# Kernel optimization log

Measured on AMD Instinct MI355X. Metric: run time of the kernel, lower is better.

The kernel has to match this reference:

```python
import jax, jax.numpy as jnp
import numpy as np

NUM_HEADS = 8
QK_DIM = 64
V_DIM = 64


def _conv1x1(W, b, x):
    # W: [out, in], x: [N, in, T, V] -> [N, out, T, V]
    return jnp.einsum('oc,nctv->notv', W, x) + b[None, :, None, None]


def setup_inputs() -> dict:
    key = jax.random.key(0)
    ks = jax.random.split(key, 10)
    N, C, T, V = 8, 256, 1024, 25
    s = 0.02
    return {
        'feature': jax.random.normal(ks[0], (N, C, T, V), jnp.float32),
        'text_feature': jax.random.normal(ks[1], (1, 512, 1, V), jnp.float32),
        'Wq': jax.random.normal(ks[2], (NUM_HEADS * QK_DIM, 512), jnp.float32) * s,
        'bq': jax.random.normal(ks[3], (NUM_HEADS * QK_DIM,), jnp.float32) * s,
        'Wk': jax.random.normal(ks[4], (NUM_HEADS * QK_DIM, 512), jnp.float32) * s,
        'bk': jax.random.normal(ks[5], (NUM_HEADS * QK_DIM,), jnp.float32) * s,
        'Wv': jax.random.normal(ks[6], (V_DIM, C), jnp.float32) * s,
        'bv': jax.random.normal(ks[7], (V_DIM,), jnp.float32) * s,
        'Wo': jax.random.normal(ks[8], (C, NUM_HEADS * V_DIM), jnp.float32) * s,
        'bo': jax.random.normal(ks[9], (C,), jnp.float32) * s,
    }


def reference(feature, text_feature, Wq, bq, Wk, bk, Wv, bv, Wo, bo):
    N, C, T, V = feature.shape
    tf = jnp.broadcast_to(text_feature, (N, 512, 1, V))  # expand over batch
    # Q/K from text features (T dim collapses to 1)
    q = _conv1x1(Wq, bq, tf).reshape(N, NUM_HEADS, QK_DIM, V)
    k = _conv1x1(Wk, bk, tf).reshape(N, NUM_HEADS, QK_DIM, V)
    v = _conv1x1(Wv, bv, feature)  # [N, v_dim, T, V]
    energy = jnp.einsum('nhcu,nhcv->nhuv', q, k) / jnp.sqrt(jnp.float32(QK_DIM))
    attn = jax.nn.softmax(energy, axis=-1)  # [N, H, V, V]
    z = jnp.einsum('nctu,nhuv->nhctv', v, attn).reshape(N, NUM_HEADS * V_DIM, T, V)
    out = _conv1x1(Wo, bo, z) + feature
    return out
```

## Files before the change

kernel.cpp:

```cpp
#include <hip/hip_runtime.h>
#include <hip/hip_bf16.h>


typedef __attribute__((ext_vector_type(8))) short short8;
typedef __attribute__((ext_vector_type(4))) float f4v;

static __device__ __forceinline__ unsigned short f2bf(float f) {
  union { float f; unsigned u; } v; v.f = f;
  unsigned r = v.u + 0x7fffu + ((v.u >> 16) & 1u);
  return (unsigned short)(r >> 16);
}
static __device__ __forceinline__ float bf2f(unsigned short h) {
  union { unsigned u; float f; } v; v.u = ((unsigned)h) << 16;
  return v.f;
}


__global__ void k_qk_conv(const float* __restrict__ tf,
                          const float* __restrict__ Wq, const float* __restrict__ bq,
                          const float* __restrict__ Wk, const float* __restrict__ bk,
                          const float* __restrict__ Wv, const float* __restrict__ Wo,
                          unsigned short* __restrict__ WvP,
                          unsigned short* __restrict__ WoP,
                          float* __restrict__ qkP)
{
  __shared__ float tfl[12800];
  const int b = blockIdx.x, tid = threadIdx.x;
  if (b < 100) {
    for (int i = tid; i < 12800; i += 256) tfl[i] = tf[i];
    __syncthreads();
    int idx = b * 256 + tid;
    int isK = idx >= 12800;
    int j = isK ? idx - 12800 : idx;
    int g = j / 25, u = j - 25 * g;
    const float* wrow = (isK ? Wk : Wq) + g * 512;
    float s = (isK ? bk : bq)[g];
    for (int i = 0; i < 512; ++i) s += wrow[i] * tfl[i * 25 + u];
    qkP[idx] = s;
  } else {
    int cb = b - 100;
    for (int i = cb * 256 + tid; i < 16896; i += 64 * 256) {
      int c = i / 264, kk = i - 264 * c;
      WvP[i] = (kk < 256) ? f2bf(Wv[c * 256 + kk]) : (unsigned short)0;
    }
    for (int i = cb * 256 + tid; i < 147456; i += 64 * 256) {
      int hh = i / 18432, rr = i - 18432 * hh;
      int o = rr / 72, kk = rr - 72 * o;
      WoP[i] = (kk < 64) ? f2bf(Wo[o * 512 + hh * 64 + kk]) : (unsigned short)0;
    }
  }
}

__global__ void k_attn(const float* __restrict__ qkP,
                       unsigned short* __restrict__ attnP)
{
  __shared__ float ql[1600], kl[1600], attl[625];
  const int h = blockIdx.x, tid = threadIdx.x;
  for (int i = tid; i < 1600; i += 256) {
    ql[i] = qkP[h * 1600 + i];
    kl[i] = qkP[12800 + h * 1600 + i];
  }
  __syncthreads();
  if (tid < 25) {
    int u = tid;
    float e[25];
    float mx = -1e30f;
    #pragma unroll
    for (int v = 0; v < 25; ++v) {
      float s = 0.f;
      #pragma unroll
      for (int r = 0; r < 64; ++r) s += ql[r * 25 + u] * kl[r * 25 + v];
      s *= 0.125f;
      e[v] = s;
      mx = fmaxf(mx, s);
    }
    float den = 0.f;
    #pragma unroll
    for (int v = 0; v < 25; ++v) { e[v] = __expf(e[v] - mx); den += e[v]; }
    float inv = 1.f / den;
    #pragma unroll
    for (int v = 0; v < 25; ++v) attl[u * 25 + v] = e[v] * inv;
  }
  __syncthreads();
  for (int i = tid; i < 1280; i += 256) {
    int vp = i / 40, u = i - 40 * vp;
    attnP[h * 1280 + i] =
        (vp < 25 && u < 25) ? f2bf(attl[u * 25 + vp]) : (unsigned short)0;
  }
}

__launch_bounds__(512, 2)
__global__ void k_main(const float* __restrict__ feature,
                       const float* __restrict__ bv,
                       const float* __restrict__ bo,
                       const unsigned short* __restrict__ WvP,
                       const unsigned short* __restrict__ WoP,
                       const unsigned short* __restrict__ attnP,
                       float* __restrict__ out)
{
  extern __shared__ char smem[];
  unsigned short* Fl = (unsigned short*)smem;
  unsigned short* Vl = (unsigned short*)(smem + 67584);
  unsigned short* Zl = (unsigned short*)(smem + 84992);
  unsigned short* Wl = (unsigned short*)(smem + 103424);

  const int tid  = threadIdx.x;
  const int wave = tid >> 6;
  const int lane = tid & 63;
  const int quad = lane >> 4;
  const int l16  = lane & 15;
  const int n  = blockIdx.x >> 8;
  const int tb = blockIdx.x & 255;
  const int t0 = tb * 4;

  {
    short8 z = {0, 0, 0, 0, 0, 0, 0, 0};
    short8* fz = (short8*)smem;
    for (int i = tid; i < 4224; i += 512) fz[i] = z;
  }
  __syncthreads();

  {
    const int c = tid >> 1, p = tid & 1;
    const float4* src = reinterpret_cast<const float4*>(
        feature + ((size_t)(n * 256 + c) * 1024 + t0) * 25);
    for (int i = p; i < 25; i += 2) {
      float4 f = src[i];
      float vv[4] = {f.x, f.y, f.z, f.w};
      int j0 = 4 * i;
      #pragma unroll
      for (int e = 0; e < 4; ++e) {
        int j = j0 + e;
        int t = j / 25;
        int vp = j - 25 * t;
        Fl[(t * 32 + vp) * 264 + c] = f2bf(vv[e]);
      }
    }
  }
  __syncthreads();

  const int wm = wave >> 1, wn = wave & 1;

  f4v acc[4][4];
  #pragma unroll
  for (int mi = 0; mi < 4; ++mi) {
    #pragma unroll
    for (int r = 0; r < 4; ++r) {
      int o = wm * 64 + mi * 16 + quad * 4 + r;
      float bor = bo[o];
      #pragma unroll
      for (int ni = 0; ni < 4; ++ni) {
        int colb = wn * 64 + ni * 16 + l16;
        acc[mi][ni][r] = bor + bf2f(Fl[colb * 264 + o]);
      }
    }
  }

  {
    const int mt1 = wave & 3, nh1 = wave >> 2;
    f4v accv[4];
    #pragma unroll
    for (int ni = 0; ni < 4; ++ni) {
      #pragma unroll
      for (int r = 0; r < 4; ++r) accv[ni][r] = bv[mt1 * 16 + quad * 4 + r];
    }
    #pragma unroll
    for (int ks = 0; ks < 8; ++ks) {
      short8 a = *reinterpret_cast<const short8*>(
          WvP + (mt1 * 16 + l16) * 264 + ks * 32 + quad * 8);
      #pragma unroll
      for (int ni = 0; ni < 4; ++ni) {
        int colb = (4 * nh1 + ni) * 16 + l16;
        short8 b = *reinterpret_cast<const short8*>(
            &Fl[colb * 264 + ks * 32 + quad * 8]);
        accv[ni] = __builtin_amdgcn_mfma_f32_16x16x32_bf16(a, b, accv[ni], 0, 0, 0);
      }
    }
    #pragma unroll
    for (int ni = 0; ni < 4; ++ni) {
      int colb = (4 * nh1 + ni) * 16 + l16;
      #pragma unroll
      for (int r = 0; r < 4; ++r) {
        int c = mt1 * 16 + quad * 4 + r;
        Vl[c * 136 + colb] = f2bf(accv[ni][r]);
      }
    }
  }
  __syncthreads();

  #pragma unroll 1
  for (int h = 0; h < 8; ++h) {
    const short8* wsrc = reinterpret_cast<const short8*>(WoP + h * 18432);
    short8 wo_stage[5];
    #pragma unroll
    for (int c2 = 0; c2 < 5; ++c2) {
      int i = tid + c2 * 512;
      if (i < 2304) wo_stage[c2] = wsrc[i];
    }

    {
      const int t2 = wave >> 1, mh = wave & 1;
      f4v accz[2][2];
      #pragma unroll
      for (int m2 = 0; m2 < 2; ++m2) {
        #pragma unroll
        for (int n2 = 0; n2 < 2; ++n2) {
          f4v z = {0.f, 0.f, 0.f, 0.f};
          accz[m2][n2] = z;
        }
      }
      short8 bfrag[2];
      #pragma unroll
      for (int n2 = 0; n2 < 2; ++n2)
        bfrag[n2] = *reinterpret_cast<const short8*>(
            attnP + h * 1280 + (n2 * 16 + l16) * 40 + quad * 8);
      #pragma unroll
      for (int m2 = 0; m2 < 2; ++m2) {
        short8 a = *reinterpret_cast<const short8*>(
            &Vl[((2 * mh + m2) * 16 + l16) * 136 + t2 * 32 + quad * 8]);
        #pragma unroll
        for (int n2 = 0; n2 < 2; ++n2)
          accz[m2][n2] =
              __builtin_amdgcn_mfma_f32_16x16x32_bf16(a, bfrag[n2], accz[m2][n2], 0, 0, 0);
      }
      #pragma unroll
      for (int m2 = 0; m2 < 2; ++m2) {
        #pragma unroll
        for (int n2 = 0; n2 < 2; ++n2) {
          #pragma unroll
          for (int r = 0; r < 4; ++r) {
            int c = (2 * mh + m2) * 16 + quad * 4 + r;
            int colz = t2 * 32 + n2 * 16 + l16;
            Zl[colz * 72 + c] = f2bf(accz[m2][n2][r]);
          }
        }
      }
    }

    {
      short8* wdst = reinterpret_cast<short8*>(Wl);
      #pragma unroll
      for (int c2 = 0; c2 < 5; ++c2) {
        int i = tid + c2 * 512;
        if (i < 2304) wdst[i] = wo_stage[c2];
      }
    }
    __syncthreads();

    #pragma unroll
    for (int ks = 0; ks < 2; ++ks) {
      short8 afr[4], bfr[4];
      #pragma unroll
      for (int mi = 0; mi < 4; ++mi)
        afr[mi] = *reinterpret_cast<const short8*>(
            &Wl[(wm * 64 + mi * 16 + l16) * 72 + ks * 32 + quad * 8]);
      #pragma unroll
      for (int ni = 0; ni < 4; ++ni)
        bfr[ni] = *reinterpret_cast<const short8*>(
            &Zl[(wn * 64 + ni * 16 + l16) * 72 + ks * 32 + quad * 8]);
      #pragma unroll
      for (int mi = 0; mi < 4; ++mi) {
        #pragma unroll
        for (int ni = 0; ni < 4; ++ni)
          acc[mi][ni] =
              __builtin_amdgcn_mfma_f32_16x16x32_bf16(afr[mi], bfr[ni], acc[mi][ni], 0, 0, 0);
      }
    }
    __syncthreads();
  }

  #pragma unroll
  for (int ni = 0; ni < 4; ++ni) {
    int colb = wn * 64 + ni * 16 + l16;
    int t = colb >> 5, vp = colb & 31;
    if (vp < 25) {
      #pragma unroll
      for (int mi = 0; mi < 4; ++mi) {
        #pragma unroll
        for (int r = 0; r < 4; ++r) {
          int o = wm * 64 + mi * 16 + quad * 4 + r;
          out[((size_t)(n * 256 + o) * 1024 + (t0 + t)) * 25 + vp] = acc[mi][ni][r];
        }
      }
    }
  }
}

extern "C" void kernel_launch(void* const* d_in, const int* in_sizes, int n_in,
                              void* d_out, int out_size, void* d_ws, size_t ws_size,
                              hipStream_t stream)
{
  const float* feature = (const float*)d_in[0];
  const float* tf      = (const float*)d_in[1];
  const float* Wq      = (const float*)d_in[2];
  const float* bq      = (const float*)d_in[3];
  const float* Wk      = (const float*)d_in[4];
  const float* bk      = (const float*)d_in[5];
  const float* Wv      = (const float*)d_in[6];
  const float* bv      = (const float*)d_in[7];
  const float* Wo      = (const float*)d_in[8];
  const float* bo      = (const float*)d_in[9];
  float* out = (float*)d_out;

  unsigned short* WvP   = (unsigned short*)d_ws;
  unsigned short* WoP   = WvP + 16896;
  unsigned short* attnP = WoP + 147456;
  float* qkP = (float*)(attnP + 10240);

  hipLaunchKernelGGL(k_qk_conv, dim3(164), dim3(256), 0, stream,
                     tf, Wq, bq, Wk, bk, Wv, Wo, WvP, WoP, qkP);
  hipLaunchKernelGGL(k_attn, dim3(8), dim3(256), 0, stream, qkP, attnP);

  hipFuncSetAttribute(reinterpret_cast<const void*>(&k_main),
                      hipFuncAttributeMaxDynamicSharedMemorySize, 140288);
  hipLaunchKernelGGL(k_main, dim3(2048), dim3(512), 140288, stream,
                     feature, bv, bo, WvP, WoP, attnP, out);
}
```

Measured before the change: 551.2 us.

## Halve per-block time tile and read Wo fragments straight from global

The main kernel now processes 2 time steps per block instead of 4, doubling the grid and shrinking LDS use from about 140KB to about 52KB so more blocks can be resident per CU (launch bounds raised to 6). The per-head Wo staging through shared memory is removed and the MFMA A fragments are loaded directly from the packed bf16 Wo in global/L2, with padding dropped from the Wv/Wo packed layouts. This aims to raise occupancy and remove an LDS copy and its register staging. In exchange, Wo is re-read from cache by twice as many blocks, and the unpadded global loads rely on L2 bandwidth.

```diff
diff --git a/kernel.cpp b/kernel.cpp
--- a/kernel.cpp
+++ b/kernel.cpp
@@ -3,6 +3,7 @@
 
 
 typedef __attribute__((ext_vector_type(8))) short short8;
+typedef __attribute__((ext_vector_type(4))) short short4v;
 typedef __attribute__((ext_vector_type(4))) float f4v;
 
 static __device__ __forceinline__ unsigned short f2bf(float f) {
@@ -39,14 +40,13 @@
     qkP[idx] = s;
   } else {
     int cb = b - 100;
-    for (int i = cb * 256 + tid; i < 16896; i += 64 * 256) {
-      int c = i / 264, kk = i - 264 * c;
-      WvP[i] = (kk < 256) ? f2bf(Wv[c * 256 + kk]) : (unsigned short)0;
-    }
-    for (int i = cb * 256 + tid; i < 147456; i += 64 * 256) {
-      int hh = i / 18432, rr = i - 18432 * hh;
-      int o = rr / 72, kk = rr - 72 * o;
-      WoP[i] = (kk < 64) ? f2bf(Wo[o * 512 + hh * 64 + kk]) : (unsigned short)0;
+    for (int i = cb * 256 + tid; i < 16384; i += 64 * 256) {
+      WvP[i] = f2bf(Wv[i]);
+    }
+    for (int i = cb * 256 + tid; i < 131072; i += 64 * 256) {
+      int hh = i >> 14, rr = i & 16383;
+      int o = rr >> 6, kk = rr & 63;
+      WoP[i] = f2bf(Wo[o * 512 + hh * 64 + kk]);
     }
   }
 }
@@ -89,7 +89,7 @@
   }
 }
 
-__launch_bounds__(512, 2)
+__launch_bounds__(512, 6)
 __global__ void k_main(const float* __restrict__ feature,
                        const float* __restrict__ bv,
                        const float* __restrict__ bo,
@@ -100,57 +100,54 @@
 {
   extern __shared__ char smem[];
   unsigned short* Fl = (unsigned short*)smem;
-  unsigned short* Vl = (unsigned short*)(smem + 67584);
-  unsigned short* Zl = (unsigned short*)(smem + 84992);
-  unsigned short* Wl = (unsigned short*)(smem + 103424);
+  unsigned short* Vl = (unsigned short*)(smem + 33792);
+  unsigned short* Zl = (unsigned short*)(smem + 43008);
 
   const int tid  = threadIdx.x;
   const int wave = tid >> 6;
   const int lane = tid & 63;
   const int quad = lane >> 4;
   const int l16  = lane & 15;
-  const int n  = blockIdx.x >> 8;
-  const int tb = blockIdx.x & 255;
-  const int t0 = tb * 4;
+  const int n  = blockIdx.x >> 9;
+  const int tb = blockIdx.x & 511;
+  const int t0 = tb * 2;
 
   {
     short8 z = {0, 0, 0, 0, 0, 0, 0, 0};
     short8* fz = (short8*)smem;
-    for (int i = tid; i < 4224; i += 512) fz[i] = z;
+    for (int i = tid; i < 2112; i += 512) fz[i] = z;
   }
   __syncthreads();
 
   {
     const int c = tid >> 1, p = tid & 1;
-    const float4* src = reinterpret_cast<const float4*>(
+    const float2* src = reinterpret_cast<const float2*>(
         feature + ((size_t)(n * 256 + c) * 1024 + t0) * 25);
     for (int i = p; i < 25; i += 2) {
-      float4 f = src[i];
-      float vv[4] = {f.x, f.y, f.z, f.w};
-      int j0 = 4 * i;
-      #pragma unroll
-      for (int e = 0; e < 4; ++e) {
-        int j = j0 + e;
-        int t = j / 25;
-        int vp = j - 25 * t;
-        Fl[(t * 32 + vp) * 264 + c] = f2bf(vv[e]);
-      }
-    }
-  }
-  __syncthreads();
-
-  const int wm = wave >> 1, wn = wave & 1;
-
-  f4v acc[4][4];
+      float2 f = src[i];
+      int j0 = 2 * i;
+      {
+        int j = j0;       int t = (j >= 25); int vp = j - 25 * t;
+        Fl[(t * 32 + vp) * 264 + c] = f2bf(f.x);
+      }
+      {
+        int j = j0 + 1;   int t = (j >= 25); int vp = j - 25 * t;
+        Fl[(t * 32 + vp) * 264 + c] = f2bf(f.y);
+      }
+    }
+  }
+  __syncthreads();
+
+  f4v acc[2][4];
   #pragma unroll
-  for (int mi = 0; mi < 4; ++mi) {
+  for (int mi = 0; mi < 2; ++mi) {
     #pragma unroll
     for (int r = 0; r < 4; ++r) {
-      int o = wm * 64 + mi * 16 + quad * 4 + r;
+      int o = wave * 32 + mi * 16 + quad * 4 + r;
       float bor = bo[o];
       #pragma unroll
       for (int ni = 0; ni < 4; ++ni) {
-        int colb = wn * 64 + ni * 16 + l16;
+        int colb = ni * 16 + l16;
         acc[mi][ni][r] = bor + bf2f(Fl[colb * 264 + o]);
       }
     }
@@ -158,31 +155,31 @@
 
   {
     const int mt1 = wave & 3, nh1 = wave >> 2;
-    f4v accv[4];
-    #pragma unroll
-    for (int ni = 0; ni < 4; ++ni) {
+    f4v accv[2];
+    #pragma unroll
+    for (int ni = 0; ni < 2; ++ni) {
       #pragma unroll
       for (int r = 0; r < 4; ++r) accv[ni][r] = bv[mt1 * 16 + quad * 4 + r];
     }
     #pragma unroll
     for (int ks = 0; ks < 8; ++ks) {
       short8 a = *reinterpret_cast<const short8*>(
-          WvP + (mt1 * 16 + l16) * 264 + ks * 32 + quad * 8);
-      #pragma unroll
-      for (int ni = 0; ni < 4; ++ni) {
-        int colb = (4 * nh1 + ni) * 16 + l16;
+          WvP + (mt1 * 16 + l16) * 256 + ks * 32 + quad * 8);
+      #pragma unroll
+      for (int ni = 0; ni < 2; ++ni) {
+        int colb = (2 * nh1 + ni) * 16 + l16;
         short8 b = *reinterpret_cast<const short8*>(
             &Fl[colb * 264 + ks * 32 + quad * 8]);
         accv[ni] = __builtin_amdgcn_mfma_f32_16x16x32_bf16(a, b, accv[ni], 0, 0, 0);
       }
     }
     #pragma unroll
-    for (int ni = 0; ni < 4; ++ni) {
-      int colb = (4 * nh1 + ni) * 16 + l16;
+    for (int ni = 0; ni < 2; ++ni) {
+      int colb = (2 * nh1 + ni) * 16 + l16;
       #pragma unroll
       for (int r = 0; r < 4; ++r) {
         int c = mt1 * 16 + quad * 4 + r;
-        Vl[c * 136 + colb] = f2bf(accv[ni][r]);
+        Vl[c * 72 + colb] = f2bf(accv[ni][r]);
       }
     }
   }
@@ -190,80 +187,51 @@
 
   #pragma unroll 1
   for (int h = 0; h < 8; ++h) {
-    const short8* wsrc = reinterpret_cast<const short8*>(WoP + h * 18432);
-    short8 wo_stage[5];
-    #pragma unroll
-    for (int c2 = 0; c2 < 5; ++c2) {
-      int i = tid + c2 * 512;
-      if (i < 2304) wo_stage[c2] = wsrc[i];
-    }
-
     {
-      const int t2 = wave >> 1, mh = wave & 1;
-      f4v accz[2][2];
-      #pragma unroll
-      for (int m2 = 0; m2 < 2; ++m2) {
-        #pragma unroll
-        for (int n2 = 0; n2 < 2; ++n2) {
-          f4v z = {0.f, 0.f, 0.f, 0.f};
-          accz[m2][n2] = z;
+      const int am = wave >> 1;
+      const int np = wave & 1;
+      short8 a = *reinterpret_cast<const short8*>(
+          &Vl[(am * 16 + l16) * 72 + np * 32 + quad * 8]);
+      f4v accz[2];
+      #pragma unroll
+      for (int j = 0; j < 2; ++j) {
+        f4v z = {0.f, 0.f, 0.f, 0.f};
+        short8 b = *reinterpret_cast<const short8*>(
+            attnP + h * 1280 + (j * 16 + l16) * 40 + quad * 8);
+        accz[j] = __builtin_amdgcn_mfma_f32_16x16x32_bf16(a, b, z, 0, 0, 0);
+      }
+      #pragma unroll
+      for (int j = 0; j < 2; ++j) {
+        int col = np * 32 + j * 16 + l16;
+        int c0 = am * 16 + quad * 4;
+        short4v zz;
+        #pragma unroll
+        for (int r = 0; r < 4; ++r) zz[r] = (short)f2bf(accz[j][r]);
+        *reinterpret_cast<short4v*>(&Zl[col * 72 + c0]) = zz;
+      }
+    }
+    __syncthreads();
+
+    {
+      const unsigned short* __restrict__ woh = WoP + h * 16384;
+      #pragma unroll
+      for (int ks = 0; ks < 2; ++ks) {
+        short8 bfr[4], afr[2];
+        #pragma unroll
+        for (int ni = 0; ni < 4; ++ni)
+          bfr[ni] = *reinterpret_cast<const short8*>(
+              &Zl[(ni * 16 + l16) * 72 + ks * 32 + quad * 8]);
+        #pragma unroll
+        for (int mi = 0; mi < 2; ++mi)
+          afr[mi] = *reinterpret_cast<const short8*>(
+              woh + (wave * 32 + mi * 16 + l16) * 64 + ks * 32 + quad * 8);
+        #pragma unroll
+        for (int mi = 0; mi < 2; ++mi) {
+          #pragma unroll
+          for (int ni = 0; ni < 4; ++ni)
+            acc[mi][ni] =
+                __builtin_amdgcn_mfma_f32_16x16x32_bf16(afr[mi], bfr[ni], acc[mi][ni], 0, 0, 0);
         }
-      }
-      short8 bfrag[2];
-      #pragma unroll
-      for (int n2 = 0; n2 < 2; ++n2)
-        bfrag[n2] = *reinterpret_cast<const short8*>(
-            attnP + h * 1280 + (n2 * 16 + l16) * 40 + quad * 8);
-      #pragma unroll
-      for (int m2 = 0; m2 < 2; ++m2) {
-        short8 a = *reinterpret_cast<const short8*>(
-            &Vl[((2 * mh + m2) * 16 + l16) * 136 + t2 * 32 + quad * 8]);
-        #pragma unroll
-        for (int n2 = 0; n2 < 2; ++n2)
-          accz[m2][n2] =
-              __builtin_amdgcn_mfma_f32_16x16x32_bf16(a, bfrag[n2], accz[m2][n2], 0, 0, 0);
-      }
-      #pragma unroll
-      for (int m2 = 0; m2 < 2; ++m2) {
-        #pragma unroll
-        for (int n2 = 0; n2 < 2; ++n2) {
-          #pragma unroll
-          for (int r = 0; r < 4; ++r) {
-            int c = (2 * mh + m2) * 16 + quad * 4 + r;
-            int colz = t2 * 32 + n2 * 16 + l16;
-            Zl[colz * 72 + c] = f2bf(accz[m2][n2][r]);
-          }
-        }
-      }
-    }
-
-    {
-      short8* wdst = reinterpret_cast<short8*>(Wl);
-      #pragma unroll
-      for (int c2 = 0; c2 < 5; ++c2) {
-        int i = tid + c2 * 512;
-        if (i < 2304) wdst[i] = wo_stage[c2];
-      }
-    }
-    __syncthreads();
-
-    #pragma unroll
-    for (int ks = 0; ks < 2; ++ks) {
-      short8 afr[4], bfr[4];
-      #pragma unroll
-      for (int mi = 0; mi < 4; ++mi)
-        afr[mi] = *reinterpret_cast<const short8*>(
-            &Wl[(wm * 64 + mi * 16 + l16) * 72 + ks * 32 + quad * 8]);
-      #pragma unroll
-      for (int ni = 0; ni < 4; ++ni)
-        bfr[ni] = *reinterpret_cast<const short8*>(
-            &Zl[(wn * 64 + ni * 16 + l16) * 72 + ks * 32 + quad * 8]);
-      #pragma unroll
-      for (int mi = 0; mi < 4; ++mi) {
-        #pragma unroll
-        for (int ni = 0; ni < 4; ++ni)
-          acc[mi][ni] =
-              __builtin_amdgcn_mfma_f32_16x16x32_bf16(afr[mi], bfr[ni], acc[mi][ni], 0, 0, 0);
       }
     }
     __syncthreads();
@@ -271,14 +239,14 @@
 
   #pragma unroll
   for (int ni = 0; ni < 4; ++ni) {
-    int colb = wn * 64 + ni * 16 + l16;
+    int colb = ni * 16 + l16;
     int t = colb >> 5, vp = colb & 31;
     if (vp < 25) {
       #pragma unroll
-      for (int mi = 0; mi < 4; ++mi) {
+      for (int mi = 0; mi < 2; ++mi) {
         #pragma unroll
         for (int r = 0; r < 4; ++r) {
-          int o = wm * 64 + mi * 16 + quad * 4 + r;
+          int o = wave * 32 + mi * 16 + quad * 4 + r;
           out[((size_t)(n * 256 + o) * 1024 + (t0 + t)) * 25 + vp] = acc[mi][ni][r];
         }
       }
@@ -303,16 +271,14 @@
   float* out = (float*)d_out;
 
   unsigned short* WvP   = (unsigned short*)d_ws;
-  unsigned short* WoP   = WvP + 16896;
-  unsigned short* attnP = WoP + 147456;
+  unsigned short* WoP   = WvP + 16384;
+  unsigned short* attnP = WoP + 131072;
   float* qkP = (float*)(attnP + 10240);
 
   hipLaunchKernelGGL(k_qk_conv, dim3(164), dim3(256), 0, stream,
                      tf, Wq, bq, Wk, bk, Wv, Wo, WvP, WoP, qkP);
   hipLaunchKernelGGL(k_attn, dim3(8), dim3(256), 0, stream, qkP, attnP);
 
-  hipFuncSetAttribute(reinterpret_cast<const void*>(&k_main),
-                      hipFuncAttributeMaxDynamicSharedMemorySize, 140288);
-  hipLaunchKernelGGL(k_main, dim3(2048), dim3(512), 140288, stream,
+  hipLaunchKernelGGL(k_main, dim3(4096), dim3(512), 52224, stream,
                      feature, bv, bo, WvP, WoP, attnP, out);
 }
```

New measurement: 593.8 us. +7.7%, slower.
